# Kernel tuning notes

Measured on AMD Instinct MI355X. Metric: run time of the kernel, lower is better.

## Reference

```python
import jax, jax.numpy as jnp
import numpy as np

IN_FEATURES = 4096
OUT_FEATURES = 4096
BATCH = 4096
MAX_STATES = 100.0
THRESHOLD = MAX_STATES * 0.2  # 20.0


def setup_inputs() -> dict:
    key = jax.random.key(0)
    k1, k2 = jax.random.split(key)
    spike_input = jax.random.uniform(k1, (BATCH, IN_FEATURES), dtype=jnp.float32)
    # synapse_states ~ N(0,1)*20 + threshold, clamped to [-max, max] (as in __init__)
    states = jax.random.normal(k2, (OUT_FEATURES, IN_FEATURES), dtype=jnp.float32) * 20.0 + THRESHOLD
    synapse_states = jnp.clip(states, -MAX_STATES, MAX_STATES)
    membrane_potential = jnp.zeros((OUT_FEATURES,), dtype=jnp.float32)
    adaptive_threshold = jnp.full((OUT_FEATURES,), 2.0, dtype=jnp.float32)
    refractory_count = jnp.zeros((OUT_FEATURES,), dtype=jnp.float32)
    return {
        "spike_input": spike_input,
        "synapse_states": synapse_states,
        "membrane_potential": membrane_potential,
        "adaptive_threshold": adaptive_threshold,
        "refractory_count": refractory_count,
    }


def reference(spike_input, synapse_states, membrane_potential, adaptive_threshold, refractory_count):
    # Ternary weights: +1 if state > thr, -1 if state < -thr, else 0
    w = jnp.where(synapse_states > THRESHOLD, 1.0,
                  jnp.where(synapse_states < -THRESHOLD, -1.0, 0.0)).astype(spike_input.dtype)
    # current: [B, out] = x [B, in] @ w.T [in, out]
    current = jnp.einsum('bi,oi->bo', spike_input, w)
    is_refractory = (refractory_count > 0).astype(current.dtype)[None, :]  # [1, out]
    effective_current = current * (1.0 - is_refractory)
    new_v_mem = membrane_potential[None, :] * 0.5 + effective_current      # [B, out]
    spikes = (new_v_mem >= adaptive_threshold[None, :]).astype(current.dtype)
    return spikes
```

## Files before the change

### kernel.cpp

```cpp
#include <hip/hip_runtime.h>


#define K_DIM 4096
#define N_OUT 4096
#define B_DIM 4096
#define BK 64

typedef __attribute__((ext_vector_type(4))) int i32x4;
typedef __attribute__((ext_vector_type(4))) float float4v;

#define AS1 __attribute__((address_space(1)))
#define AS3 __attribute__((address_space(3)))

__global__ __launch_bounds__(256) void prep_kernel(
    const float* __restrict__ X, const float* __restrict__ S,
    unsigned int* __restrict__ Xq, unsigned int* __restrict__ Wq)
{
    const int i = blockIdx.x * 256 + threadIdx.x;
    float4v x = ((const float4v*)X)[i];
    float4v s = ((const float4v*)S)[i];
    unsigned int xw = 0, ww = 0;
#pragma unroll
    for (int j = 0; j < 4; ++j) {
        unsigned int xb = (unsigned int)(int)(x[j] * 127.0f + 0.5f) & 0xFFu;
        int wv = (s[j] > 20.0f) ? 1 : ((s[j] < -20.0f) ? -1 : 0);
        unsigned int wb = (unsigned int)wv & 0xFFu;
        xw |= xb << (8 * j);
        ww |= wb << (8 * j);
    }
    Xq[i] = xw;
    Wq[i] = ww;
}


#define STAGE2(SBUF, KTS, PH) do {                                            \
    if ((PH) == 0) {                                                          \
        __builtin_amdgcn_global_load_lds((const AS1 void*)(pA0 + (KTS)),      \
            (AS3 void*)(lds + (SBUF) * 32768 + dst0), 16, 0, 0);              \
        __builtin_amdgcn_global_load_lds((const AS1 void*)(pA1 + (KTS)),      \
            (AS3 void*)(lds + (SBUF) * 32768 + dst1), 16, 0, 0);              \
    } else {                                                                  \
        __builtin_amdgcn_global_load_lds((const AS1 void*)(pB0 + (KTS)),      \
            (AS3 void*)(lds + (SBUF) * 32768 + 16384 + dst0), 16, 0, 0);      \
        __builtin_amdgcn_global_load_lds((const AS1 void*)(pB1 + (KTS)),      \
            (AS3 void*)(lds + (SBUF) * 32768 + 16384 + dst1), 16, 0, 0);      \
    } } while (0)

#define ITER(RBUF, SBUF, DO_STAGE, WAITN) do {                                \
    const char* base = lds + (RBUF) * 32768;                                  \
    i32x4 a[4], b[4];                                                         \
    _Pragma("unroll")                                                         \
    for (int n = 0; n < 4; ++n) b[n] = *(const i32x4*)(base + sB + n * 1024); \
    _Pragma("unroll")                                                         \
    for (int m = 0; m < 4; ++m) a[m] = *(const i32x4*)(base + sA + m * 1024); \
    if (DO_STAGE) STAGE2(SBUF, kts, 0);                                       \
    asm volatile("s_barrier" ::: "memory");                                   \
    __builtin_amdgcn_s_setprio(1);                                            \
    _Pragma("unroll")                                                         \
    for (int m = 0; m < 4; ++m)                                               \
        _Pragma("unroll")                                                     \
        for (int n = 0; n < 4; ++n)                                           \
            acc[m][n] = __builtin_amdgcn_mfma_i32_16x16x64_i8(                \
                a[m], b[n], acc[m][n], 0, 0, 0);                              \
    __builtin_amdgcn_s_setprio(0);                                            \
    asm volatile("s_barrier" ::: "memory");                                   \
    _Pragma("unroll")                                                         \
    for (int m = 0; m < 4; ++m)                                               \
        a[m] = *(const i32x4*)(base + sA + 4096 + m * 1024);                  \
    if (DO_STAGE) STAGE2(SBUF, kts, 1);                                       \
    asm volatile("s_barrier" ::: "memory");                                   \
    __builtin_amdgcn_s_setprio(1);                                            \
    _Pragma("unroll")                                                         \
    for (int m = 0; m < 4; ++m)                                               \
        _Pragma("unroll")                                                     \
        for (int n = 0; n < 4; ++n)                                           \
            acc[m + 4][n] = __builtin_amdgcn_mfma_i32_16x16x64_i8(            \
                a[m], b[n], acc[m + 4][n], 0, 0, 0);                          \
    __builtin_amdgcn_s_setprio(0);                                            \
    asm volatile("s_waitcnt vmcnt(" #WAITN ")" ::: "memory");                 \
    asm volatile("s_barrier" ::: "memory");                                   \
    kts += BK;                                                                \
} while (0)

__global__ __launch_bounds__(512, 2) void snn_gemm8(
    const char* __restrict__ Xq,
    const char* __restrict__ Wq,
    const float* __restrict__ vmem,
    const float* __restrict__ thr,
    const float* __restrict__ refr,
    float* __restrict__ out)
{
    extern __shared__ char lds[];

    const int tid  = threadIdx.x;
    const int lane = tid & 63;
    const int wid  = tid >> 6;
    const int wr   = wid >> 2;
    const int wcol = wid & 3;
    const int fr   = lane & 15;
    const int fq   = lane >> 4;

    const int bid  = blockIdx.y * gridDim.x + blockIdx.x;
    const int swzb = (bid & 7) * 32 + (bid >> 3);
    const int bm = (swzb & 15) * 256;
    const int bn = (swzb >> 4) * 256;

    const int swz16 = (fq ^ ((fr >> 1) & 3)) << 4;
    const int sA = wr * 8192 + fr * 64 + swz16;
    const int sB = 16384 + wcol * 4096 + fr * 64 + swz16;

    int rowS[2], colS[2];
#pragma unroll
    for (int r = 0; r < 2; ++r) {
        int o  = (r * 512 + tid) * 16;
        int os = o ^ (((o >> 7) & 3) << 4);
        rowS[r] = os >> 6;
        colS[r] = os & 63;
    }
    const char* pA0 = Xq + (size_t)(bm + rowS[0]) * K_DIM + colS[0];
    const char* pA1 = Xq + (size_t)(bm + rowS[1]) * K_DIM + colS[1];
    const char* pB0 = Wq + (size_t)(bn + rowS[0]) * K_DIM + colS[0];
    const char* pB1 = Wq + (size_t)(bn + rowS[1]) * K_DIM + colS[1];
    const int dst0 = tid * 16;
    const int dst1 = tid * 16 + 8192;

    i32x4 acc[8][4] = {};

    STAGE2(0, 0, 0);   STAGE2(0, 0, 1);
    STAGE2(1, 64, 0);  STAGE2(1, 64, 1);
    STAGE2(2, 128, 0); STAGE2(2, 128, 1);
    asm volatile("s_waitcnt vmcnt(8)" ::: "memory");
    asm volatile("s_barrier" ::: "memory");

    int kts = 192;

#pragma unroll 1
    for (int tt = 0; tt < 15; ++tt) {
        ITER(0, 3, 1, 8);
        ITER(1, 0, 1, 8);
        ITER(2, 1, 1, 8);
        ITER(3, 2, 1, 8);
    }
    ITER(0, 3, 1, 8);
    ITER(1, 0, 0, 4);
    ITER(2, 0, 0, 0);
    ITER(3, 0, 0, 0);

    const float inv127 = 1.0f / 127.0f;
#pragma unroll
    for (int n = 0; n < 4; ++n) {
        const int gc = bn + wcol * 64 + n * 16 + fr;
        const bool refract = refr[gc] > 0.0f;
        const float tv = thr[gc];
        const float vm = vmem[gc] * 0.5f;
#pragma unroll
        for (int m = 0; m < 8; ++m) {
            const int gr = bm + wr * 128 + m * 16 + fq * 4;
#pragma unroll
            for (int j = 0; j < 4; ++j) {
                const float cur = refract ? 0.0f : (float)acc[m][n][j] * inv127;
                out[(size_t)(gr + j) * N_OUT + gc] = (vm + cur >= tv) ? 1.0f : 0.0f;
            }
        }
    }
}

extern "C" void kernel_launch(void* const* d_in, const int* in_sizes, int n_in,
                              void* d_out, int out_size, void* d_ws, size_t ws_size,
                              hipStream_t stream) {
    const float* X    = (const float*)d_in[0];
    const float* S    = (const float*)d_in[1];
    const float* vmem = (const float*)d_in[2];
    const float* thr  = (const float*)d_in[3];
    const float* refr = (const float*)d_in[4];
    float* out = (float*)d_out;

    char* Xq = (char*)d_ws;
    char* Wq = (char*)d_ws + (size_t)B_DIM * K_DIM;

    prep_kernel<<<(B_DIM * K_DIM) / 4 / 256, 256, 0, stream>>>(
        X, S, (unsigned int*)Xq, (unsigned int*)Wq);

    hipFuncSetAttribute((const void*)snn_gemm8,
                        hipFuncAttributeMaxDynamicSharedMemorySize, 131072);
    dim3 grid(B_DIM / 256, N_OUT / 256);
    snn_gemm8<<<grid, 512, 131072, stream>>>(Xq, Wq, vmem, thr, refr, out);
}
```

Measured before the change: 234.9 us.

## Shrink GEMM tile to 128x128 with 4 waves and 3-stage LDS ring

Replaces the 256x256 block tile (8 waves, 4-stage 32KB buffers, split A-half phases) with a 128x128 tile using 4 waves, a 3-stage 16KB LDS ring, and a single staging phase per k-step. Launches 1024 blocks instead of 256 with up to 3 blocks per CU, aiming for better load balance across CUs and fewer barriers per iteration. The trade-off is lower data reuse per block, so more global/L2 traffic for X and W, and fewer MFMAs between barriers.

```diff
diff --git a/kernel.cpp b/kernel.cpp
--- a/kernel.cpp
+++ b/kernel.cpp
@@ -5,6 +5,7 @@
 #define N_OUT 4096
 #define B_DIM 4096
 #define BK 64
+#define BUFSZ 16384
 
 typedef __attribute__((ext_vector_type(4))) int i32x4;
 typedef __attribute__((ext_vector_type(4))) float float4v;
@@ -24,36 +25,33 @@
     for (int j = 0; j < 4; ++j) {
         unsigned int xb = (unsigned int)(int)(x[j] * 127.0f + 0.5f) & 0xFFu;
         int wv = (s[j] > 20.0f) ? 1 : ((s[j] < -20.0f) ? -1 : 0);
-        unsigned int wb = (unsigned int)wv & 0xFFu;
         xw |= xb << (8 * j);
-        ww |= wb << (8 * j);
+        ww |= ((unsigned int)wv & 0xFFu) << (8 * j);
     }
     Xq[i] = xw;
     Wq[i] = ww;
 }
 
 
-#define STAGE2(SBUF, KTS, PH) do {                                            \
-    if ((PH) == 0) {                                                          \
-        __builtin_amdgcn_global_load_lds((const AS1 void*)(pA0 + (KTS)),      \
-            (AS3 void*)(lds + (SBUF) * 32768 + dst0), 16, 0, 0);              \
-        __builtin_amdgcn_global_load_lds((const AS1 void*)(pA1 + (KTS)),      \
-            (AS3 void*)(lds + (SBUF) * 32768 + dst1), 16, 0, 0);              \
-    } else {                                                                  \
-        __builtin_amdgcn_global_load_lds((const AS1 void*)(pB0 + (KTS)),      \
-            (AS3 void*)(lds + (SBUF) * 32768 + 16384 + dst0), 16, 0, 0);      \
-        __builtin_amdgcn_global_load_lds((const AS1 void*)(pB1 + (KTS)),      \
-            (AS3 void*)(lds + (SBUF) * 32768 + 16384 + dst1), 16, 0, 0);      \
-    } } while (0)
+#define STAGE(SB, KTS) do {                                                   \
+    __builtin_amdgcn_global_load_lds((const AS1 void*)(pA0 + (KTS)),          \
+        (AS3 void*)(lds + (SB) * BUFSZ + dstA0), 16, 0, 0);                   \
+    __builtin_amdgcn_global_load_lds((const AS1 void*)(pA1 + (KTS)),          \
+        (AS3 void*)(lds + (SB) * BUFSZ + dstA1), 16, 0, 0);                   \
+    __builtin_amdgcn_global_load_lds((const AS1 void*)(pB0 + (KTS)),          \
+        (AS3 void*)(lds + (SB) * BUFSZ + dstB0), 16, 0, 0);                   \
+    __builtin_amdgcn_global_load_lds((const AS1 void*)(pB1 + (KTS)),          \
+        (AS3 void*)(lds + (SB) * BUFSZ + dstB1), 16, 0, 0);                   \
+} while (0)
 
 #define ITER(RBUF, SBUF, DO_STAGE, WAITN) do {                                \
-    const char* base = lds + (RBUF) * 32768;                                  \
+    const char* base = lds + (RBUF) * BUFSZ;                                  \
     i32x4 a[4], b[4];                                                         \
     _Pragma("unroll")                                                         \
     for (int n = 0; n < 4; ++n) b[n] = *(const i32x4*)(base + sB + n * 1024); \
     _Pragma("unroll")                                                         \
     for (int m = 0; m < 4; ++m) a[m] = *(const i32x4*)(base + sA + m * 1024); \
-    if (DO_STAGE) STAGE2(SBUF, kts, 0);                                       \
+    if (DO_STAGE) STAGE(SBUF, kts);                                           \
     asm volatile("s_barrier" ::: "memory");                                   \
     __builtin_amdgcn_s_setprio(1);                                            \
     _Pragma("unroll")                                                         \
@@ -63,26 +61,12 @@
             acc[m][n] = __builtin_amdgcn_mfma_i32_16x16x64_i8(                \
                 a[m], b[n], acc[m][n], 0, 0, 0);                              \
     __builtin_amdgcn_s_setprio(0);                                            \
-    asm volatile("s_barrier" ::: "memory");                                   \
-    _Pragma("unroll")                                                         \
-    for (int m = 0; m < 4; ++m)                                               \
-        a[m] = *(const i32x4*)(base + sA + 4096 + m * 1024);                  \
-    if (DO_STAGE) STAGE2(SBUF, kts, 1);                                       \
-    asm volatile("s_barrier" ::: "memory");                                   \
-    __builtin_amdgcn_s_setprio(1);                                            \
-    _Pragma("unroll")                                                         \
-    for (int m = 0; m < 4; ++m)                                               \
-        _Pragma("unroll")                                                     \
-        for (int n = 0; n < 4; ++n)                                           \
-            acc[m + 4][n] = __builtin_amdgcn_mfma_i32_16x16x64_i8(            \
-                a[m], b[n], acc[m + 4][n], 0, 0, 0);                          \
-    __builtin_amdgcn_s_setprio(0);                                            \
     asm volatile("s_waitcnt vmcnt(" #WAITN ")" ::: "memory");                 \
     asm volatile("s_barrier" ::: "memory");                                   \
     kts += BK;                                                                \
 } while (0)
 
-__global__ __launch_bounds__(512, 2) void snn_gemm8(
+__global__ __launch_bounds__(256, 3) void snn_gemm4(
     const char* __restrict__ Xq,
     const char* __restrict__ Wq,
     const float* __restrict__ vmem,
@@ -95,56 +79,56 @@
     const int tid  = threadIdx.x;
     const int lane = tid & 63;
     const int wid  = tid >> 6;
-    const int wr   = wid >> 2;
-    const int wcol = wid & 3;
+    const int wr   = wid >> 1;
+    const int wcol = wid & 1;
     const int fr   = lane & 15;
     const int fq   = lane >> 4;
 
     const int bid  = blockIdx.y * gridDim.x + blockIdx.x;
-    const int swzb = (bid & 7) * 32 + (bid >> 3);
-    const int bm = (swzb & 15) * 256;
-    const int bn = (swzb >> 4) * 256;
+    const int swzb = (bid & 7) * 128 + (bid >> 3);
+    const int bm = (swzb & 31) * 128;
+    const int bn = (swzb >> 5) * 128;
 
     const int swz16 = (fq ^ ((fr >> 1) & 3)) << 4;
-    const int sA = wr * 8192 + fr * 64 + swz16;
-    const int sB = 16384 + wcol * 4096 + fr * 64 + swz16;
+    const int sA = wr * 4096 + fr * 64 + swz16;
+    const int sB = 8192 + wcol * 4096 + fr * 64 + swz16;
 
-    int rowS[2], colS[2];
+    int rowS[4], colS[4];
 #pragma unroll
-    for (int r = 0; r < 2; ++r) {
-        int o  = (r * 512 + tid) * 16;
+    for (int r = 0; r < 4; ++r) {
+        int o  = (r & 1) * 4096 + tid * 16;
         int os = o ^ (((o >> 7) & 3) << 4);
         rowS[r] = os >> 6;
         colS[r] = os & 63;
     }
     const char* pA0 = Xq + (size_t)(bm + rowS[0]) * K_DIM + colS[0];
     const char* pA1 = Xq + (size_t)(bm + rowS[1]) * K_DIM + colS[1];
-    const char* pB0 = Wq + (size_t)(bn + rowS[0]) * K_DIM + colS[0];
-    const char* pB1 = Wq + (size_t)(bn + rowS[1]) * K_DIM + colS[1];
-    const int dst0 = tid * 16;
-    const int dst1 = tid * 16 + 8192;
+    const char* pB0 = Wq + (size_t)(bn + rowS[2]) * K_DIM + colS[2];
+    const char* pB1 = Wq + (size_t)(bn + rowS[3]) * K_DIM + colS[3];
+    const int dstA0 = tid * 16;
+    const int dstA1 = 4096 + tid * 16;
+    const int dstB0 = 8192 + tid * 16;
+    const int dstB1 = 12288 + tid * 16;
 
-    i32x4 acc[8][4] = {};
+    i32x4 acc[4][4] = {};
 
-    STAGE2(0, 0, 0);   STAGE2(0, 0, 1);
-    STAGE2(1, 64, 0);  STAGE2(1, 64, 1);
-    STAGE2(2, 128, 0); STAGE2(2, 128, 1);
-    asm volatile("s_waitcnt vmcnt(8)" ::: "memory");
+    STAGE(0, 0);
+    STAGE(1, 64);
+    asm volatile("s_waitcnt vmcnt(4)" ::: "memory");
     asm volatile("s_barrier" ::: "memory");
 
-    int kts = 192;
+    int kts = 128;
 
 #pragma unroll 1
-    for (int tt = 0; tt < 15; ++tt) {
-        ITER(0, 3, 1, 8);
-        ITER(1, 0, 1, 8);
-        ITER(2, 1, 1, 8);
-        ITER(3, 2, 1, 8);
+    for (int tt = 0; tt < 20; ++tt) {
+        ITER(0, 2, 1, 4);
+        ITER(1, 0, 1, 4);
+        ITER(2, 1, 1, 4);
     }
-    ITER(0, 3, 1, 8);
-    ITER(1, 0, 0, 4);
+    ITER(0, 2, 1, 4);
+    ITER(1, 0, 1, 4);
     ITER(2, 0, 0, 0);
-    ITER(3, 0, 0, 0);
+    ITER(0, 0, 0, 0);
 
     const float inv127 = 1.0f / 127.0f;
 #pragma unroll
@@ -154,8 +138,8 @@
         const float tv = thr[gc];
         const float vm = vmem[gc] * 0.5f;
 #pragma unroll
-        for (int m = 0; m < 8; ++m) {
-            const int gr = bm + wr * 128 + m * 16 + fq * 4;
+        for (int m = 0; m < 4; ++m) {
+            const int gr = bm + wr * 64 + m * 16 + fq * 4;
 #pragma unroll
             for (int j = 0; j < 4; ++j) {
                 const float cur = refract ? 0.0f : (float)acc[m][n][j] * inv127;
@@ -181,8 +165,8 @@
     prep_kernel<<<(B_DIM * K_DIM) / 4 / 256, 256, 0, stream>>>(
         X, S, (unsigned int*)Xq, (unsigned int*)Wq);
 
-    hipFuncSetAttribute((const void*)snn_gemm8,
-                        hipFuncAttributeMaxDynamicSharedMemorySize, 131072);
-    dim3 grid(B_DIM / 256, N_OUT / 256);
-    snn_gemm8<<<grid, 512, 131072, stream>>>(Xq, Wq, vmem, thr, refr, out);
+    hipFuncSetAttribute((const void*)snn_gemm4,
+                        hipFuncAttributeMaxDynamicSharedMemorySize, 49152);
+    dim3 grid(B_DIM / 128, N_OUT / 128);
+    snn_gemm4<<<grid, 256, 49152, stream>>>(Xq, Wq, vmem, thr, refr, out);
 }
```

New measurement: 263.4 us. 1.12x slower.
